# Kernel tuning notes

Measured on AMD Instinct MI355X. Metric: run time of the kernel, lower is better.

Reference implementation:

```python
import jax, jax.numpy as jnp
import numpy as np

H, W, C, B = 64, 64, 512, 16

def _dwconv(x, w, b, k):
    # x: [B,C,H,W]; w: [C,1,k,k] depthwise kernel; b: [C]
    pad = k // 2
    out = jax.lax.conv_general_dilated(
        x, w, window_strides=(1, 1), padding=[(pad, pad), (pad, pad)],
        dimension_numbers=('NCHW', 'OIHW', 'NCHW'), feature_group_count=x.shape[1])
    return out + b[None, :, None, None]

def setup_inputs() -> dict:
    key = jax.random.key(0)
    ks = jax.random.split(key, 7)
    x = jax.random.normal(ks[0], (B, 1 + H * W, C), dtype=jnp.float32)
    def kinit(k, ksize):
        fan_in = ksize * ksize  # groups=C -> in_ch per group = 1
        bound = 1.0 / np.sqrt(fan_in)
        return jax.random.uniform(k, (C, 1, ksize, ksize), jnp.float32, -bound, bound)
    w7 = kinit(ks[1], 7); b7 = jax.random.uniform(ks[2], (C,), jnp.float32, -1/7.0, 1/7.0)
    w5 = kinit(ks[3], 5); b5 = jax.random.uniform(ks[4], (C,), jnp.float32, -1/5.0, 1/5.0)
    w3 = kinit(ks[5], 3); b3 = jax.random.uniform(ks[6], (C,), jnp.float32, -1/3.0, 1/3.0)
    return {'x': x, 'w7': w7, 'b7': b7, 'w5': w5, 'b5': b5, 'w3': w3, 'b3': b3}

def reference(x, w7, b7, w5, b5, w3, b3):
    Bn, N, Cn = x.shape
    cls_token = x[:, 0]          # [B, C]
    feat_token = x[:, 1:]        # [B, H*W, C]
    cnn_feat = feat_token.transpose(0, 2, 1).reshape(Bn, Cn, H, W)
    y = (_dwconv(cnn_feat, w7, b7, 7) + cnn_feat
         + _dwconv(cnn_feat, w5, b5, 5)
         + _dwconv(cnn_feat, w3, b3, 3))
    y = y.reshape(Bn, Cn, H * W).transpose(0, 2, 1)   # [B, HW, C]
    return jnp.concatenate([cls_token[:, None, :], y], axis=1)
```

## Files before the change

kernel.cpp:

```cpp
#include <hip/hip_runtime.h>

#define Hh 64
#define Ww 64
#define Cc 512
#define Bb 16
#define NTOK (1 + Hh * Ww)
#define TW 8
#define TH 8

__global__ void ppeg_prep(const float* __restrict__ w7, const float* __restrict__ b7,
                          const float* __restrict__ w5, const float* __restrict__ b5,
                          const float* __restrict__ w3, const float* __restrict__ b3,
                          const float* __restrict__ x, float* __restrict__ wt,
                          float* __restrict__ beff, float* __restrict__ out) {
    int idx = blockIdx.x * blockDim.x + threadIdx.x;
    if (idx < Cc * 49) {
        int c = idx / 49, t = idx % 49;
        int r = t / 7, s = t % 7;
        float v = w7[idx];
        if (r >= 1 && r <= 5 && s >= 1 && s <= 5) v += w5[c * 25 + (r - 1) * 5 + (s - 1)];
        if (r >= 2 && r <= 4 && s >= 2 && s <= 4) v += w3[c * 9 + (r - 2) * 3 + (s - 2)];
        if (t == 24) v += 1.0f;
        wt[t * Cc + c] = v;
    }
    if (idx < Cc) beff[idx] = b7[idx] + b5[idx] + b3[idx];
    if (idx < Bb * Cc) {
        int b = idx / Cc, c = idx % Cc;
        size_t o = (size_t)b * NTOK * Cc + c;
        out[o] = x[o];
    }
}

__global__ __launch_bounds__(256, 2)
void ppeg_conv(const float* __restrict__ x, const float* __restrict__ wt,
               const float* __restrict__ beff, float* __restrict__ out) {
    const int tx = threadIdx.x;
    const int ty = threadIdx.y;
    const int c  = blockIdx.y * 64 + tx;
    const int b  = blockIdx.z;
    const int wblk = blockIdx.x & 7;
    const int hblk = blockIdx.x >> 3;
    const int oh0   = hblk * 32 + ty * TH;
    const int wbase = wblk * TW;

    const float* xb = x + ((size_t)b * NTOK + 1) * Cc + c;

    float tap[49];
#pragma unroll
    for (int t = 0; t < 49; ++t) tap[t] = wt[t * Cc + c];

    const float bias = beff[c];
    float acc[TH][TW];
#pragma unroll
    for (int o = 0; o < TH; ++o)
#pragma unroll
        for (int j = 0; j < TW; ++j) acc[o][j] = bias;

    const bool interior = (wblk != 0) && (wblk != 7);

#pragma unroll
    for (int k = 0; k < TH + 6; ++k) {
        const int ir = oh0 + k - 3;
        if (ir >= 0 && ir < Hh) {
            const float* xrow = xb + (size_t)ir * (Ww * Cc);
            float v[TW + 6];
            if (interior) {
#pragma unroll
                for (int j = 0; j < TW + 6; ++j)
                    v[j] = xrow[(size_t)(wbase - 3 + j) * Cc];
            } else {
#pragma unroll
                for (int j = 0; j < TW + 6; ++j) {
                    const int wc = wbase + j - 3;
                    v[j] = (wc >= 0 && wc < Ww) ? xrow[(size_t)wc * Cc] : 0.0f;
                }
            }
#pragma unroll
            for (int o = 0; o < TH; ++o) {
                if (o > k || o < k - 6) continue;
                const int r = k - o;
#pragma unroll
                for (int s = 0; s < 7; ++s) {
                    const float tp = tap[r * 7 + s];
#pragma unroll
                    for (int j = 0; j < TW; ++j)
                        acc[o][j] = fmaf(tp, v[j + s], acc[o][j]);
                }
            }
        }
    }

#pragma unroll
    for (int o = 0; o < TH; ++o) {
        float* orow = out + ((size_t)b * NTOK + 1 + (size_t)(oh0 + o) * Ww + wbase) * Cc + c;
#pragma unroll
        for (int j = 0; j < TW; ++j)
            __builtin_nontemporal_store(acc[o][j], &orow[(size_t)j * Cc]);
    }
}

extern "C" void kernel_launch(void* const* d_in, const int* in_sizes, int n_in,
                              void* d_out, int out_size, void* d_ws, size_t ws_size,
                              hipStream_t stream) {
    const float* x  = (const float*)d_in[0];
    const float* w7 = (const float*)d_in[1];
    const float* b7 = (const float*)d_in[2];
    const float* w5 = (const float*)d_in[3];
    const float* b5 = (const float*)d_in[4];
    const float* w3 = (const float*)d_in[5];
    const float* b3 = (const float*)d_in[6];
    float* out = (float*)d_out;

    float* wt   = (float*)d_ws;
    float* beff = wt + 49 * Cc;

    ppeg_prep<<<(Cc * 49 + 255) / 256, 256, 0, stream>>>(w7, b7, w5, b5, w3, b3,
                                                         x, wt, beff, out);

    dim3 grid(16, Cc / 64, Bb);
    dim3 block(64, 4);
    ppeg_conv<<<grid, block, 0, stream>>>(x, wt, beff, out);
}
```

Baseline: 285.6 us.

## Remap block tiling with swizzled block order and shared-memory taps

Block-to-work mapping is rewritten so a linearized, XCD-style swizzled block index picks batch, channel group and spatial tile. The four warps of a block now sit side by side along width (32 columns) instead of stacked along height, so neighbouring warps share halo rows and columns. Filter taps move from 49 registers per thread into a shared-memory array, which lowers register pressure at the cost of LDS reads inside the inner loop and one __syncthreads per block. The swizzle aims to keep adjacent tiles on the same L2/XCD for better halo reuse.

```diff
diff --git a/kernel.cpp b/kernel.cpp
--- a/kernel.cpp
+++ b/kernel.cpp
@@ -34,20 +34,31 @@
 __global__ __launch_bounds__(256, 2)
 void ppeg_conv(const float* __restrict__ x, const float* __restrict__ wt,
                const float* __restrict__ beff, float* __restrict__ out) {
+#pragma clang fp contract(fast)
     const int tx = threadIdx.x;
     const int ty = threadIdx.y;
-    const int c  = blockIdx.y * 64 + tx;
-    const int b  = blockIdx.z;
-    const int wblk = blockIdx.x & 7;
-    const int hblk = blockIdx.x >> 3;
-    const int oh0   = hblk * 32 + ty * TH;
-    const int wbase = wblk * TW;
 
+    const int L     = blockIdx.x + 16 * (blockIdx.y + 8 * blockIdx.z);
+    const int g_lin = (L & 7) * 256 + (L >> 3);
+    const int sp    = g_lin & 15;
+    const int g     = g_lin >> 4;
+    const int cb    = (g & 7) * 64;
+    const int b     = g >> 3;
+
+    const int wtile = sp & 1;
+    const int hblk  = sp >> 1;
+    const int oh0   = hblk * TH;
+    const int wbase = wtile * 32 + ty * TW;
+
+    __shared__ float taps[49][64];
+    const int tid = ty * 64 + tx;
+    for (int idx = tid; idx < 49 * 64; idx += 256) {
+        taps[idx >> 6][idx & 63] = wt[(idx >> 6) * Cc + cb + (idx & 63)];
+    }
+    __syncthreads();
+
+    const int c = cb + tx;
     const float* xb = x + ((size_t)b * NTOK + 1) * Cc + c;
-
-    float tap[49];
-#pragma unroll
-    for (int t = 0; t < 49; ++t) tap[t] = wt[t * Cc + c];
 
     const float bias = beff[c];
     float acc[TH][TW];
@@ -56,7 +67,7 @@
 #pragma unroll
         for (int j = 0; j < TW; ++j) acc[o][j] = bias;
 
-    const bool interior = (wblk != 0) && (wblk != 7);
+    const bool interior = (wbase != 0) && (wbase != Ww - TW);
 
 #pragma unroll
     for (int k = 0; k < TH + 6; ++k) {
@@ -81,7 +92,7 @@
                 const int r = k - o;
 #pragma unroll
                 for (int s = 0; s < 7; ++s) {
-                    const float tp = tap[r * 7 + s];
+                    const float tp = taps[r * 7 + s][tx];
 #pragma unroll
                     for (int j = 0; j < TW; ++j)
                         acc[o][j] = fmaf(tp, v[j + s], acc[o][j]);
```

After: 517.2 us. +81.1%, slower.
